# Kernel optimization log

Hardware: AMD Instinct MI355X
Metric: run time of the kernel (lower is better)

## Reference

```python
import jax, jax.numpy as jnp
import numpy as np

DIM = 2048
N_HEADS = 16
HEAD_DIM = DIM // N_HEADS
ROPE_BASE = 10000.0


def _rope_cos_sin(seq_len, head_dim, dtype):
    inv_freq = 1.0 / (ROPE_BASE ** (jnp.arange(0, head_dim, 2, dtype=jnp.float32) / head_dim))
    t = jnp.arange(seq_len, dtype=jnp.float32)
    freqs = jnp.einsum('s,d->sd', t, inv_freq)          # (S, hd/2)
    emb = jnp.concatenate([freqs, freqs], axis=-1)       # (S, hd)
    return jnp.cos(emb).astype(dtype), jnp.sin(emb).astype(dtype)


def _rotate_half(x):
    x1, x2 = jnp.split(x, 2, axis=-1)
    return jnp.concatenate([-x2, x1], axis=-1)


def _apply_rope(x, cos, sin):
    # x: (B, H, S, hd); cos/sin: (S, hd)
    return x * cos[None, None] + _rotate_half(x) * sin[None, None]


def setup_inputs() -> dict:
    key = jax.random.key(0)
    ks = jax.random.split(key, 5)
    B, S = 2, 2048
    scale = 1.0 / np.sqrt(DIM)
    return {
        'x': jax.random.normal(ks[0], (B, S, DIM), dtype=jnp.float32),
        'Wq': jax.random.normal(ks[1], (DIM, DIM), dtype=jnp.float32) * scale,
        'Wk': jax.random.normal(ks[2], (DIM, DIM), dtype=jnp.float32) * scale,
        'Wv': jax.random.normal(ks[3], (DIM, DIM), dtype=jnp.float32) * scale,
        'Wo': jax.random.normal(ks[4], (DIM, DIM), dtype=jnp.float32) * scale,
    }


def reference(x, Wq, Wk, Wv, Wo):
    B, S, _ = x.shape
    scale = HEAD_DIM ** -0.5

    def proj(W):
        # torch Linear: x @ W.T ; reshape to (B, H, S, hd)
        return (x @ W.T).reshape(B, S, N_HEADS, HEAD_DIM).transpose(0, 2, 1, 3)

    q, k, v = proj(Wq), proj(Wk), proj(Wv)
    cos, sin = _rope_cos_sin(S, HEAD_DIM, x.dtype)
    q = _apply_rope(q, cos, sin)
    k = _apply_rope(k, cos, sin)

    scores = jnp.einsum('bhqd,bhkd->bhqk', q, k) * scale  # (B,H,S,S)
    causal = jnp.triu(jnp.ones((S, S), dtype=bool), k=1)
    scores = jnp.where(causal[None, None], -jnp.inf, scores)
    attn = jax.nn.softmax(scores.astype(jnp.float32), axis=-1).astype(q.dtype)
    out = jnp.einsum('bhqk,bhkd->bhqd', attn, v)          # (B,H,S,hd)
    out = out.transpose(0, 2, 1, 3).reshape(B, S, DIM)
    return out @ Wo.T
```

## Files before the change

kernel.cpp:

```cpp
#include <hip/hip_runtime.h>


#define SEQ 2048
#define DMODEL 2048
#define NH 16
#define HD 128

typedef __attribute__((ext_vector_type(8))) short bf16x8;
typedef __attribute__((ext_vector_type(4))) float f32x4;

__device__ __forceinline__ unsigned short f2bf(float f) {
  unsigned int u = __float_as_uint(f);
  u += 0x7fffu + ((u >> 16) & 1u);
  return (unsigned short)(u >> 16);
}

__device__ __forceinline__ void g2l16(const void* g, void* l) {
  __builtin_amdgcn_global_load_lds((const __attribute__((address_space(1))) void*)g,
                                   (__attribute__((address_space(3))) void*)l,
                                   16, 0, 0);
}

__device__ __forceinline__ f32x4 mfma16(bf16x8 a, bf16x8 b, f32x4 c) {
  return __builtin_amdgcn_mfma_f32_16x16x32_bf16(a, b, c, 0, 0, 0);
}

template <int CTRL>
__device__ __forceinline__ float dpp_ror(float v) {
  return __int_as_float(__builtin_amdgcn_mov_dpp(__float_as_int(v), CTRL, 0xf, 0xf, false));
}
__device__ __forceinline__ float red_max16(float v) {
  v = fmaxf(v, dpp_ror<0x128>(v));
  v = fmaxf(v, dpp_ror<0x124>(v));
  v = fmaxf(v, dpp_ror<0x122>(v));
  v = fmaxf(v, dpp_ror<0x121>(v));
  return v;
}
__device__ __forceinline__ float red_sum16(float v) {
  v += dpp_ror<0x128>(v);
  v += dpp_ror<0x124>(v);
  v += dpp_ror<0x122>(v);
  v += dpp_ror<0x121>(v);
  return v;
}

__global__ __launch_bounds__(256) void cvt_all(const float* __restrict__ x,
                                               const float* __restrict__ wq,
                                               const float* __restrict__ wk,
                                               const float* __restrict__ wv,
                                               const float* __restrict__ wo,
                                               unsigned short* __restrict__ dst0,
                                               float2* __restrict__ rtab) {
  const int b = blockIdx.x;
  if (b >= 24576) {
    const int idx = (b - 24576) * 256 + threadIdx.x;
    const int s = idx >> 6, d = idx & 63;
    float sn, cs;
    sincosf((float)s * exp2f(-0.20762050593046f * (float)d), &sn, &cs);
    rtab[idx] = make_float2(cs, sn);
    return;
  }
  const float* src;
  unsigned short* dst;
  int idx, r = -1;
  if (b < 8192) {
    src = x; dst = dst0; idx = b * 256 + threadIdx.x;
  } else {
    r = (b - 8192) >> 12;
    src = (r == 0) ? wq : (r == 1) ? wk : (r == 2) ? wv : wo;
    dst = dst0 + (size_t)2 * SEQ * DMODEL + (size_t)r * DMODEL * DMODEL;
    idx = ((b - 8192) & 4095) * 256 + threadIdx.x;
  }
  const float4 v = ((const float4*)src)[idx];
  ushort4 o;
  o.x = f2bf(v.x); o.y = f2bf(v.y); o.z = f2bf(v.z); o.w = f2bf(v.w);
  int widx = idx;
  if (r == 0 || r == 1) {
    const int row = idx >> 9, col = idx & 511;
    const int o_ = row & 127;
    const int e = (((o_ >> 4) & 3) << 5) | (((o_ >> 6) & 1) << 4) | (o_ & 15);
    widx = (((row & ~127) | e) << 9) | col;
  }
  ((ushort4*)dst)[widx] = o;
}

template <int MODE>
__global__ __launch_bounds__(512, 2) void gemm_pipe(
    const unsigned short* __restrict__ A,
    const unsigned short* __restrict__ B,
    unsigned short* __restrict__ obf,
    float* __restrict__ of32,
    const float2* __restrict__ rtab) {
  __shared__ unsigned short lds[3 * 24576];
  const int nb = blockIdx.x, mb = blockIdx.y;
  const int M0 = mb * 256;
  const int t = threadIdx.x;
  const int w = t >> 6, lane = t & 63, l15 = lane & 15, quad = lane >> 4;
  const int g = lane >> 3, j = lane & 7;
  const int wm = w >> 1, wn = w & 1;

  const unsigned short* Abase = A + (size_t)M0 * DMODEL;
  const unsigned short* Bbase = B + (size_t)nb * 128 * DMODEL;

  f32x4 acc[4][4] = {};

  auto stage = [&](int buf, int k0, int i0) {
#pragma unroll
    for (int i = 0; i < 3; ++i) {
      const int u = w * 6 + i0 + i;
      if (u < 32) {
        const int row = u * 8 + g;
        g2l16(Abase + (size_t)row * DMODEL + k0 + ((j ^ g) << 3),
              &lds[buf * 24576 + u * 512]);
      } else {
        const int row = (u - 32) * 8 + g;
        g2l16(Bbase + (size_t)row * DMODEL + k0 + ((j ^ g) << 3),
              &lds[buf * 24576 + 16384 + (u - 32) * 512]);
      }
    }
  };

  auto comp = [&](int buf, int kc) {
    const int c = kc * 4 + quad;
    const unsigned short* As_ = &lds[buf * 24576];
    const unsigned short* Bs_ = &lds[buf * 24576 + 16384];
    bf16x8 af[4], bf[4];
#pragma unroll
    for (int mt = 0; mt < 4; ++mt) {
      const int m = wm * 64 + mt * 16 + l15;
      af[mt] = *(const bf16x8*)&As_[m * 64 + ((c ^ (m & 7)) << 3)];
    }
#pragma unroll
    for (int nt = 0; nt < 4; ++nt) {
      const int n = wn * 64 + nt * 16 + l15;
      bf[nt] = *(const bf16x8*)&Bs_[n * 64 + ((c ^ (n & 7)) << 3)];
    }
#pragma unroll
    for (int nt = 0; nt < 4; ++nt)
#pragma unroll
      for (int mt = 0; mt < 4; ++mt)
        acc[mt][nt] = mfma16(af[mt], bf[nt], acc[mt][nt]);
  };

  stage(0, 0, 0);
  stage(0, 0, 3);
  stage(1, 64, 0);
  stage(1, 64, 3);
  asm volatile("s_waitcnt vmcnt(6)\n\ts_barrier" ::: "memory");

  int buf = 0, b2 = 2;
  for (int tt = 0; tt < 32; ++tt) {
    const int k0 = tt * 64;
    if (tt < 30) stage(b2, k0 + 128, 0);
    comp(buf, 0);
    if (tt < 30) stage(b2, k0 + 128, 3);
    comp(buf, 1);
    if (tt < 30) {
      asm volatile("s_waitcnt vmcnt(6)\n\ts_barrier" ::: "memory");
    } else if (tt == 30) {
      asm volatile("s_waitcnt vmcnt(0)\n\ts_barrier" ::: "memory");
    }
    buf = (buf == 2) ? 0 : buf + 1;
    b2 = (b2 == 2) ? 0 : b2 + 1;
  }

  if (MODE == 0) {
    const size_t NX = (size_t)2 * SEQ * DMODEL;
    const int z = nb >> 4;
    const int h = nb & 15;
    if (z < 2) {
      const float qscale = (z == 0) ? 0.1275174356f : 1.0f;
      unsigned short* O = obf + (size_t)z * NX;
#pragma unroll
      for (int mt = 0; mt < 4; ++mt)
#pragma unroll
        for (int reg = 0; reg < 4; ++reg) {
          const int m = M0 + wm * 64 + mt * 16 + quad * 4 + reg;
          const int bb = m >> 11, s = m & 2047;
          unsigned short* ob = O + ((size_t)(bb * NH + h) * SEQ + s) * HD;
#pragma unroll
          for (int p = 0; p < 2; ++p) {
            const int q = wn * 2 + p;
            const float2 cs = rtab[s * 64 + q * 16 + l15];
            const float x1 = acc[mt][2 * p][reg], x2 = acc[mt][2 * p + 1][reg];
            ob[wn * 64 + (2 * p) * 16 + l15] = f2bf((x1 * cs.x - x2 * cs.y) * qscale);
            ob[wn * 64 + (2 * p + 1) * 16 + l15] = f2bf((x2 * cs.x + x1 * cs.y) * qscale);
          }
        }
    } else {
      unsigned short* Vb = obf + 2 * NX + (size_t)h * HD * SEQ;
#pragma unroll
      for (int mt = 0; mt < 4; ++mt)
#pragma unroll
        for (int reg = 0; reg < 4; ++reg) {
          const int m = M0 + wm * 64 + mt * 16 + quad * 4 + reg;
          const int bb = m >> 11, s = m & 2047;
          unsigned short* ob = Vb + (size_t)bb * NH * HD * SEQ;
#pragma unroll
          for (int nt = 0; nt < 4; ++nt)
            ob[(size_t)(wn * 64 + nt * 16 + l15) * SEQ + s] = f2bf(acc[mt][nt][reg]);
        }
    }
  } else {
#pragma unroll
    for (int mt = 0; mt < 4; ++mt)
#pragma unroll
      for (int reg = 0; reg < 4; ++reg) {
        const int m = M0 + wm * 64 + mt * 16 + quad * 4 + reg;
#pragma unroll
        for (int nt = 0; nt < 4; ++nt)
          of32[(size_t)m * DMODEL + nb * 128 + wn * 64 + nt * 16 + l15] =
              acc[mt][nt][reg];
      }
  }
}

__global__ __launch_bounds__(256) void attn_kernel(const unsigned short* __restrict__ Q,
                                                   const unsigned short* __restrict__ K,
                                                   const unsigned short* __restrict__ Vt,
                                                   unsigned short* __restrict__ Oa) {
  __shared__ unsigned short Ks[2][64 * 128];
  __shared__ unsigned short Vs[2][128 * 64];
  __shared__ unsigned short Ps[4][1024];
  const int gid = blockIdx.x;
  const int bh = gid & 31;
  const int pr = gid >> 5;
  const unsigned short* Qb = Q + (size_t)bh * SEQ * HD;
  const unsigned short* Kb = K + (size_t)bh * SEQ * HD;
  const unsigned short* Vb = Vt + (size_t)bh * HD * SEQ;
  const int t = threadIdx.x;
  const int w = t >> 6, lane = t & 63, l15 = lane & 15, quad = lane >> 4;
  const int l7 = lane & 7;
  const int b = bh >> 4, h = bh & 15;
  const int uA = w * 64 + lane;

  auto stage = [&](int sb, int kt) {
    const unsigned short* Kt = Kb + (size_t)(kt * 64) * HD;
    const unsigned short* Vtk = Vb + kt * 64;
#pragma unroll
    for (int i = 0; i < 4; ++i) {
      const int u = i * 256 + uA;
      const int key = u >> 4, cs = u & 15;
      g2l16(Kt + (size_t)key * HD + ((cs ^ (key & 7)) << 3),
            &Ks[sb][(i * 256 + w * 64) * 8]);
    }
#pragma unroll
    for (int i = 0; i < 4; ++i) {
      const int u = i * 256 + uA;
      const int d = u >> 3, cs = u & 7;
      g2l16(Vtk + (size_t)d * SEQ + ((cs ^ (d & 7)) << 3),
            &Vs[sb][(i * 256 + w * 64) * 8]);
    }
  };

  for (int half = 0; half < 2; ++half) {
    const int qt = half ? 31 - pr : pr;

    bf16x8 qf[4];
#pragma unroll
    for (int ch = 0; ch < 4; ++ch)
      qf[ch] = *(const bf16x8*)(Qb + (size_t)(qt * 64 + w * 16 + l15) * HD +
                                ch * 32 + quad * 8);

    f32x4 o[8] = {};
    float mrow[4], lrow[4];
#pragma unroll
    for (int reg = 0; reg < 4; ++reg) { mrow[reg] = -1e30f; lrow[reg] = 0.f; }

    stage(0, 0);
    asm volatile("s_waitcnt vmcnt(0)\n\ts_barrier" ::: "memory");
    int buf = 0;

    for (int kt = 0; kt <= qt; ++kt) {
      if (kt < qt) stage(buf ^ 1, kt + 1);

      const bool diag = (kt == qt);
      const int ntm = diag ? w : 3;
      f32x4 s[4] = {};
      __builtin_amdgcn_s_setprio(1);
#pragma unroll
      for (int ch = 0; ch < 4; ++ch) {
        const int c = ch * 4 + quad;
#pragma unroll
        for (int nt = 0; nt < 4; ++nt) {
          if (nt <= ntm) {
            const int n = nt * 16 + l15;
            const bf16x8 bv = *(const bf16x8*)&Ks[buf][n * 128 + ((c ^ l7) << 3)];
            s[nt] = mfma16(qf[ch], bv, s[nt]);
          }
        }
      }
      __builtin_amdgcn_s_setprio(0);

      if (diag) {
#pragma unroll
        for (int nt = 0; nt < 4; ++nt)
#pragma unroll
          for (int reg = 0; reg < 4; ++reg) {
            const int rr = w * 16 + quad * 4 + reg;
            const int cc = nt * 16 + l15;
            if (cc > rr) s[nt][reg] = -1e30f;
          }
      }

#pragma unroll
      for (int reg = 0; reg < 4; ++reg) {
        float vmax = s[0][reg];
#pragma unroll
        for (int nt = 1; nt < 4; ++nt) vmax = fmaxf(vmax, s[nt][reg]);
        vmax = red_max16(vmax);
        const float mo = mrow[reg];
        float mn = mo;
        if (!__all(vmax <= mo + 8.0f)) {
          mn = fmaxf(mo, vmax);
          const float alpha = exp2f(mo - mn);
          mrow[reg] = mn;
          lrow[reg] *= alpha;
#pragma unroll
          for (int nt = 0; nt < 8; ++nt) o[nt][reg] *= alpha;
        }
        float rs = 0.f;
#pragma unroll
        for (int nt = 0; nt < 4; ++nt) {
          const float p_ = exp2f(s[nt][reg] - mn);
          s[nt][reg] = p_;
          rs += p_;
        }
        rs = red_sum16(rs);
        lrow[reg] += rs;
      }

      unsigned short* Pw = Ps[w];
#pragma unroll
      for (int nt = 0; nt < 4; ++nt)
#pragma unroll
        for (int reg = 0; reg < 4; ++reg) {
          const int key = nt * 16 + l15;
          Pw[(key >> 3) * 128 + (quad * 4 + reg) * 8 + (key & 7)] = f2bf(s[nt][reg]);
        }

      __builtin_amdgcn_s_setprio(1);
#pragma unroll
      for (int ch2 = 0; ch2 < 2; ++ch2) {
        const int c = ch2 * 4 + quad;
        const bf16x8 pa = *(const bf16x8*)&Pw[c * 128 + l15 * 8];
#pragma unroll
        for (int nt = 0; nt < 8; ++nt) {
          const int d = nt * 16 + l15;
          const bf16x8 vv = *(const bf16x8*)&Vs[buf][d * 64 + ((c ^ l7) << 3)];
          o[nt] = mfma16(pa, vv, o[nt]);
        }
      }
      __builtin_amdgcn_s_setprio(0);

      asm volatile("s_waitcnt vmcnt(0)\n\ts_barrier" ::: "memory");
      buf ^= 1;
    }

#pragma unroll
    for (int reg = 0; reg < 4; ++reg) {
      const int sq = qt * 64 + w * 16 + quad * 4 + reg;
      const float inv_l = 1.0f / lrow[reg];
      unsigned short* ob = Oa + (size_t)(b * SEQ + sq) * DMODEL + h * HD;
#pragma unroll
      for (int nt = 0; nt < 8; ++nt) ob[nt * 16 + l15] = f2bf(o[nt][reg] * inv_l);
    }
  }
}

extern "C" void kernel_launch(void* const* d_in, const int* in_sizes, int n_in,
                              void* d_out, int out_size, void* d_ws, size_t ws_size,
                              hipStream_t stream) {
  const float* x = (const float*)d_in[0];
  const float* Wq = (const float*)d_in[1];
  const float* Wk = (const float*)d_in[2];
  const float* Wv = (const float*)d_in[3];
  const float* Wo = (const float*)d_in[4];
  float* out = (float*)d_out;

  const size_t NX = (size_t)2 * SEQ * DMODEL;
  const size_t NW = (size_t)DMODEL * DMODEL;
  unsigned short* ws = (unsigned short*)d_ws;
  unsigned short* xb = ws;
  unsigned short* wqb = xb + NX;
  unsigned short* wkb = wqb + NW;
  unsigned short* wvb = wkb + NW;
  unsigned short* wob = wvb + NW;
  unsigned short* qb = wob + NW;
  unsigned short* kb = qb + NX;
  unsigned short* vb = kb + NX;
  unsigned short* ab = vb + NX;
  float2* rtab = (float2*)(ab + NX);

  cvt_all<<<25088, 256, 0, stream>>>(x, Wq, Wk, Wv, Wo, ws, rtab);
  gemm_pipe<0><<<dim3(48, 16), 512, 0, stream>>>(xb, wqb, qb, nullptr, rtab);
  attn_kernel<<<512, 256, 0, stream>>>(qb, kb, vb, ab);
  gemm_pipe<1><<<dim3(16, 16), 512, 0, stream>>>(ab, wob, nullptr, out, nullptr);
}
```

Measured before the change: 377.1 us.

## Remap GEMM blocks across XCDs and restructure pipeline with barriers and setprio

Both GEMM launches become 1D grids, and the block id is remapped so consecutive blocks scattered round-robin across the 8 XCDs share M/N tiles, aiming at better L2 locality. The k-loop is also split into phases: LDS fragment reads, then issue of the next async global-to-LDS stage, then a barrier and lgkmcnt wait, then an MFMA burst at raised wave priority. This is meant to keep the waves of a block in lockstep and favour the matrix cores. The extra barriers per iteration could add sync overhead.

```diff
diff --git a/kernel.cpp b/kernel.cpp
--- a/kernel.cpp
+++ b/kernel.cpp
@@ -92,7 +92,11 @@
     float* __restrict__ of32,
     const float2* __restrict__ rtab) {
   __shared__ unsigned short lds[3 * 24576];
-  const int nb = blockIdx.x, mb = blockIdx.y;
+  const int NBX = (MODE == 0) ? 48 : 16;
+  const int G = (MODE == 0) ? 768 : 256;
+  const int bid = blockIdx.x;
+  const int lin = (bid & 7) * (G >> 3) + (bid >> 3);
+  const int nb = lin % NBX, mb = lin / NBX;
   const int M0 = mb * 256;
   const int t = threadIdx.x;
   const int w = t >> 6, lane = t & 63, l15 = lane & 15, quad = lane >> 4;
@@ -120,11 +124,11 @@
     }
   };
 
-  auto comp = [&](int buf, int kc) {
+  auto phase = [&](int buf, int kc, bool dostage, int b2, int k2) {
     const int c = kc * 4 + quad;
     const unsigned short* As_ = &lds[buf * 24576];
     const unsigned short* Bs_ = &lds[buf * 24576 + 16384];
-    bf16x8 af[4], bf[4];
+    bf16x8 af[4], bv[4];
 #pragma unroll
     for (int mt = 0; mt < 4; ++mt) {
       const int m = wm * 64 + mt * 16 + l15;
@@ -133,13 +137,19 @@
 #pragma unroll
     for (int nt = 0; nt < 4; ++nt) {
       const int n = wn * 64 + nt * 16 + l15;
-      bf[nt] = *(const bf16x8*)&Bs_[n * 64 + ((c ^ (n & 7)) << 3)];
-    }
+      bv[nt] = *(const bf16x8*)&Bs_[n * 64 + ((c ^ (n & 7)) << 3)];
+    }
+    if (dostage) stage(b2, k2, kc * 3);
+    __builtin_amdgcn_s_barrier();
+    asm volatile("s_waitcnt lgkmcnt(0)" ::: "memory");
+    __builtin_amdgcn_sched_barrier(0);
+    __builtin_amdgcn_s_setprio(1);
 #pragma unroll
     for (int nt = 0; nt < 4; ++nt)
 #pragma unroll
       for (int mt = 0; mt < 4; ++mt)
-        acc[mt][nt] = mfma16(af[mt], bf[nt], acc[mt][nt]);
+        acc[mt][nt] = mfma16(af[mt], bv[nt], acc[mt][nt]);
+    __builtin_amdgcn_s_setprio(0);
   };
 
   stage(0, 0, 0);
@@ -150,16 +160,17 @@
 
   int buf = 0, b2 = 2;
   for (int tt = 0; tt < 32; ++tt) {
-    const int k0 = tt * 64;
-    if (tt < 30) stage(b2, k0 + 128, 0);
-    comp(buf, 0);
-    if (tt < 30) stage(b2, k0 + 128, 3);
-    comp(buf, 1);
-    if (tt < 30) {
-      asm volatile("s_waitcnt vmcnt(6)\n\ts_barrier" ::: "memory");
+    const int k2 = tt * 64 + 128;
+    const bool ds = (tt < 30);
+    phase(buf, 0, ds, b2, k2);
+    __builtin_amdgcn_s_barrier();
+    phase(buf, 1, ds, b2, k2);
+    if (ds) {
+      asm volatile("s_waitcnt vmcnt(6)" ::: "memory");
     } else if (tt == 30) {
-      asm volatile("s_waitcnt vmcnt(0)\n\ts_barrier" ::: "memory");
-    }
+      asm volatile("s_waitcnt vmcnt(0)" ::: "memory");
+    }
+    if (tt < 31) __builtin_amdgcn_s_barrier();
     buf = (buf == 2) ? 0 : buf + 1;
     b2 = (b2 == 2) ? 0 : b2 + 1;
   }
@@ -393,7 +404,7 @@
   float2* rtab = (float2*)(ab + NX);
 
   cvt_all<<<25088, 256, 0, stream>>>(x, Wq, Wk, Wv, Wo, ws, rtab);
-  gemm_pipe<0><<<dim3(48, 16), 512, 0, stream>>>(xb, wqb, qb, nullptr, rtab);
+  gemm_pipe<0><<<768, 512, 0, stream>>>(xb, wqb, qb, nullptr, rtab);
   attn_kernel<<<512, 256, 0, stream>>>(qb, kb, vb, ab);
-  gemm_pipe<1><<<dim3(16, 16), 512, 0, stream>>>(ab, wob, nullptr, out, nullptr);
-}
+  gemm_pipe<1><<<256, 512, 0, stream>>>(ab, wob, nullptr, out, nullptr);
+}
```

Result: no change. 374.3 us (-0.8%).

## Widen QKV GEMM N-tile to 192 and switch to double-buffered pipeline

Applied to the files above, without the earlier changes.

The QKV projection GEMM now uses 256x192 tiles, which cuts the grid from 768 to 512 workgroups and raises the MFMA-per-load ratio. The staging pipeline drops from triple to double buffering, waiting with vmcnt(0) each iteration, so the larger tile still fits in LDS. The epilogue is rewritten to map 32-column pairs back to the q/k/v head and RoPE positions. The costs are more accumulator registers at occupancy 2, weaker latency hiding from the shallower pipeline, and a grid of 512 blocks that may fill the CUs less evenly.

```diff
diff --git a/kernel.cpp b/kernel.cpp
--- a/kernel.cpp
+++ b/kernel.cpp
@@ -91,7 +91,12 @@
     unsigned short* __restrict__ obf,
     float* __restrict__ of32,
     const float2* __restrict__ rtab) {
-  __shared__ unsigned short lds[3 * 24576];
+  constexpr int BN = (MODE == 0) ? 192 : 128;
+  constexpr int NTW = BN / 32;
+  constexpr int TILE = (256 + BN) * 64;
+  constexpr int NU = 32 + BN / 8;
+  constexpr int UPW = NU / 8;
+  __shared__ unsigned short lds[2 * TILE];
   const int nb = blockIdx.x, mb = blockIdx.y;
   const int M0 = mb * 256;
   const int t = threadIdx.x;
@@ -100,106 +105,103 @@
   const int wm = w >> 1, wn = w & 1;
 
   const unsigned short* Abase = A + (size_t)M0 * DMODEL;
-  const unsigned short* Bbase = B + (size_t)nb * 128 * DMODEL;
-
-  f32x4 acc[4][4] = {};
-
-  auto stage = [&](int buf, int k0, int i0) {
-#pragma unroll
-    for (int i = 0; i < 3; ++i) {
-      const int u = w * 6 + i0 + i;
+  const unsigned short* Bbase = B + (size_t)nb * BN * DMODEL;
+
+  f32x4 acc[4][NTW] = {};
+
+  auto stage = [&](int buf, int k0, int i0, int i1) {
+#pragma unroll
+    for (int i = i0; i < i1; ++i) {
+      const int u = w * UPW + i;
       if (u < 32) {
-        const int row = u * 8 + g;
-        g2l16(Abase + (size_t)row * DMODEL + k0 + ((j ^ g) << 3),
-              &lds[buf * 24576 + u * 512]);
+        g2l16(Abase + (size_t)(u * 8 + g) * DMODEL + k0 + ((j ^ g) << 3),
+              &lds[buf * TILE + u * 512]);
       } else {
-        const int row = (u - 32) * 8 + g;
-        g2l16(Bbase + (size_t)row * DMODEL + k0 + ((j ^ g) << 3),
-              &lds[buf * 24576 + 16384 + (u - 32) * 512]);
+        g2l16(Bbase + (size_t)((u - 32) * 8 + g) * DMODEL + k0 + ((j ^ g) << 3),
+              &lds[buf * TILE + 16384 + (u - 32) * 512]);
       }
     }
   };
 
   auto comp = [&](int buf, int kc) {
     const int c = kc * 4 + quad;
-    const unsigned short* As_ = &lds[buf * 24576];
-    const unsigned short* Bs_ = &lds[buf * 24576 + 16384];
-    bf16x8 af[4], bf[4];
+    const unsigned short* As_ = &lds[buf * TILE];
+    const unsigned short* Bs_ = &lds[buf * TILE + 16384];
+    bf16x8 af[4], bv[NTW];
 #pragma unroll
     for (int mt = 0; mt < 4; ++mt) {
       const int m = wm * 64 + mt * 16 + l15;
       af[mt] = *(const bf16x8*)&As_[m * 64 + ((c ^ (m & 7)) << 3)];
     }
 #pragma unroll
-    for (int nt = 0; nt < 4; ++nt) {
-      const int n = wn * 64 + nt * 16 + l15;
-      bf[nt] = *(const bf16x8*)&Bs_[n * 64 + ((c ^ (n & 7)) << 3)];
-    }
-#pragma unroll
-    for (int nt = 0; nt < 4; ++nt)
+    for (int nt = 0; nt < NTW; ++nt) {
+      const int n = wn * (BN / 2) + nt * 16 + l15;
+      bv[nt] = *(const bf16x8*)&Bs_[n * 64 + ((c ^ (n & 7)) << 3)];
+    }
+#pragma unroll
+    for (int nt = 0; nt < NTW; ++nt)
 #pragma unroll
       for (int mt = 0; mt < 4; ++mt)
-        acc[mt][nt] = mfma16(af[mt], bf[nt], acc[mt][nt]);
+        acc[mt][nt] = mfma16(af[mt], bv[nt], acc[mt][nt]);
   };
 
-  stage(0, 0, 0);
-  stage(0, 0, 3);
-  stage(1, 64, 0);
-  stage(1, 64, 3);
-  asm volatile("s_waitcnt vmcnt(6)\n\ts_barrier" ::: "memory");
-
-  int buf = 0, b2 = 2;
+  stage(0, 0, 0, UPW);
+  asm volatile("s_waitcnt vmcnt(0)\n\ts_barrier" ::: "memory");
+
+  int buf = 0;
   for (int tt = 0; tt < 32; ++tt) {
-    const int k0 = tt * 64;
-    if (tt < 30) stage(b2, k0 + 128, 0);
+    const bool ps = (tt < 31);
+    if (ps) stage(buf ^ 1, tt * 64 + 64, 0, UPW / 2);
     comp(buf, 0);
-    if (tt < 30) stage(b2, k0 + 128, 3);
+    if (ps) stage(buf ^ 1, tt * 64 + 64, UPW / 2, UPW);
     comp(buf, 1);
-    if (tt < 30) {
-      asm volatile("s_waitcnt vmcnt(6)\n\ts_barrier" ::: "memory");
-    } else if (tt == 30) {
+    if (ps) {
       asm volatile("s_waitcnt vmcnt(0)\n\ts_barrier" ::: "memory");
-    }
-    buf = (buf == 2) ? 0 : buf + 1;
-    b2 = (b2 == 2) ? 0 : b2 + 1;
+      buf ^= 1;
+    }
   }
 
   if (MODE == 0) {
     const size_t NX = (size_t)2 * SEQ * DMODEL;
-    const int z = nb >> 4;
-    const int h = nb & 15;
-    if (z < 2) {
-      const float qscale = (z == 0) ? 0.1275174356f : 1.0f;
-      unsigned short* O = obf + (size_t)z * NX;
-#pragma unroll
-      for (int mt = 0; mt < 4; ++mt)
-#pragma unroll
-        for (int reg = 0; reg < 4; ++reg) {
-          const int m = M0 + wm * 64 + mt * 16 + quad * 4 + reg;
-          const int bb = m >> 11, s = m & 2047;
-          unsigned short* ob = O + ((size_t)(bb * NH + h) * SEQ + s) * HD;
-#pragma unroll
-          for (int p = 0; p < 2; ++p) {
-            const int q = wn * 2 + p;
-            const float2 cs = rtab[s * 64 + q * 16 + l15];
-            const float x1 = acc[mt][2 * p][reg], x2 = acc[mt][2 * p + 1][reg];
-            ob[wn * 64 + (2 * p) * 16 + l15] = f2bf((x1 * cs.x - x2 * cs.y) * qscale);
-            ob[wn * 64 + (2 * p + 1) * 16 + l15] = f2bf((x2 * cs.x + x1 * cs.y) * qscale);
+#pragma unroll
+    for (int pp = 0; pp < NTW / 2; ++pp) {
+      const int colb = nb * BN + wn * (BN / 2) + pp * 32;
+      const int z = colb >> 11;
+      const int zc = colb & 2047;
+      const int h = zc >> 7;
+      const int e0 = zc & 127;
+      if (z < 2) {
+        const float qscale = (z == 0) ? 0.1275174356f : 1.0f;
+        unsigned short* O = obf + (size_t)z * NX;
+        const int rt = (e0 >> 5) * 16 + l15;
+#pragma unroll
+        for (int mt = 0; mt < 4; ++mt)
+#pragma unroll
+          for (int reg = 0; reg < 4; ++reg) {
+            const int m = M0 + wm * 64 + mt * 16 + quad * 4 + reg;
+            const int bb = m >> 11, s = m & 2047;
+            unsigned short* ob = O + ((size_t)(bb * NH + h) * SEQ + s) * HD;
+            const float2 cs = rtab[s * 64 + rt];
+            const float x1 = acc[mt][2 * pp][reg], x2 = acc[mt][2 * pp + 1][reg];
+            ob[e0 + l15] = f2bf((x1 * cs.x - x2 * cs.y) * qscale);
+            ob[e0 + 16 + l15] = f2bf((x2 * cs.x + x1 * cs.y) * qscale);
           }
-        }
-    } else {
-      unsigned short* Vb = obf + 2 * NX + (size_t)h * HD * SEQ;
-#pragma unroll
-      for (int mt = 0; mt < 4; ++mt)
-#pragma unroll
-        for (int reg = 0; reg < 4; ++reg) {
-          const int m = M0 + wm * 64 + mt * 16 + quad * 4 + reg;
-          const int bb = m >> 11, s = m & 2047;
-          unsigned short* ob = Vb + (size_t)bb * NH * HD * SEQ;
-#pragma unroll
-          for (int nt = 0; nt < 4; ++nt)
-            ob[(size_t)(wn * 64 + nt * 16 + l15) * SEQ + s] = f2bf(acc[mt][nt][reg]);
-        }
+      } else {
+        unsigned short* Vb0 = obf + 2 * NX + (size_t)h * HD * SEQ;
+#pragma unroll
+        for (int q2 = 0; q2 < 2; ++q2) {
+          const int d = e0 + q2 * 16 + l15;
+#pragma unroll
+          for (int mt = 0; mt < 4; ++mt)
+#pragma unroll
+            for (int reg = 0; reg < 4; ++reg) {
+              const int m = M0 + wm * 64 + mt * 16 + quad * 4 + reg;
+              const int bb = m >> 11, s = m & 2047;
+              unsigned short* ob = Vb0 + (size_t)bb * NH * HD * SEQ;
+              ob[(size_t)d * SEQ + s] = f2bf(acc[mt][2 * pp + q2][reg]);
+            }
+        }
+      }
     }
   } else {
 #pragma unroll
@@ -208,8 +210,8 @@
       for (int reg = 0; reg < 4; ++reg) {
         const int m = M0 + wm * 64 + mt * 16 + quad * 4 + reg;
 #pragma unroll
-        for (int nt = 0; nt < 4; ++nt)
-          of32[(size_t)m * DMODEL + nb * 128 + wn * 64 + nt * 16 + l15] =
+        for (int nt = 0; nt < NTW; ++nt)
+          of32[(size_t)m * DMODEL + nb * BN + wn * (BN / 2) + nt * 16 + l15] =
               acc[mt][nt][reg];
       }
   }
@@ -393,7 +395,7 @@
   float2* rtab = (float2*)(ab + NX);
 
   cvt_all<<<25088, 256, 0, stream>>>(x, Wq, Wk, Wv, Wo, ws, rtab);
-  gemm_pipe<0><<<dim3(48, 16), 512, 0, stream>>>(xb, wqb, qb, nullptr, rtab);
+  gemm_pipe<0><<<dim3(32, 16), 512, 0, stream>>>(xb, wqb, qb, nullptr, rtab);
   attn_kernel<<<512, 256, 0, stream>>>(qb, kb, vb, ab);
   gemm_pipe<1><<<dim3(16, 16), 512, 0, stream>>>(ab, wob, nullptr, out, nullptr);
 }
```

New measurement: 356.7 us. -5.4%, faster.
